# Optimization experiments

Measured on AMD Instinct MI355X. Metric: run time of the kernel, lower is better.

The kernel has to match this reference:

```python
import jax, jax.numpy as jnp
import numpy as np


def setup_inputs() -> dict:
    key = jax.random.key(0)
    nX, time_steps, T = 1024, 256, 10
    u0 = jax.random.normal(key, (nX, nX), dtype=jnp.float32)
    # learnable scalar diffusivity; 2e-4 keeps gamma <= 0.25 (stable scheme)
    alpha = jnp.asarray(2e-4, dtype=jnp.float32)
    return {"u0": u0, "alpha": alpha, "T": T, "nX": nX, "time_steps": time_steps}


def reference(u0, alpha, T, nX, time_steps):
    delta_x = 6.0 / (nX - 1)
    delta_t = T / (time_steps - 1)
    gamma = alpha * delta_t / delta_x ** 2

    # Torch code writes u0 at t=0, then zeroes all four boundaries for every t.
    u_init = jnp.zeros_like(u0).at[1:-1, 1:-1].set(u0[1:-1, 1:-1])

    def step(u, _):
        # 5-point Laplacian stencil on the interior; boundaries stay 0
        lap = (u[2:, 1:-1] + u[:-2, 1:-1] + u[1:-1, 2:] + u[1:-1, :-2]
               - 4.0 * u[1:-1, 1:-1])
        un = jnp.zeros_like(u).at[1:-1, 1:-1].set(gamma * lap + u[1:-1, 1:-1])
        return un, un

    _, us = jax.lax.scan(step, u_init, None, length=time_steps - 1)
    # u: [time_steps, nX, nX]
    return jnp.concatenate([u_init[None], us], axis=0)
```

## Files before the change

kernel.cpp:

```cpp
#include <hip/hip_runtime.h>
#include <math.h>


#define CORE 64
#define HALO 20
#define TILE 104
#define TPB  1024
#define NQ   26
#define NIT  (102 * NQ)

#define BAR() do { \
    asm volatile("s_waitcnt lgkmcnt(0)" ::: "memory"); \
    __builtin_amdgcn_s_barrier(); \
    __builtin_amdgcn_sched_barrier(0); \
} while (0)

__device__ __forceinline__ float4 load_quad_strict(const float* __restrict__ fp,
                                                   int gr, int gc0, int nX) {
    float4 v = make_float4(0.f, 0.f, 0.f, 0.f);
    if (gr > 0 && gr < nX - 1) {
        const float* sp = fp + (size_t)gr * nX + gc0;
        if (gc0 > 0 && gc0 + 3 < nX - 1) {
            v = *reinterpret_cast<const float4*>(sp);
        } else {
            if (gc0     > 0 && gc0     < nX - 1) v.x = sp[0];
            if (gc0 + 1 > 0 && gc0 + 1 < nX - 1) v.y = sp[1];
            if (gc0 + 2 > 0 && gc0 + 2 < nX - 1) v.z = sp[2];
            if (gc0 + 3 > 0 && gc0 + 3 < nX - 1) v.w = sp[3];
        }
    }
    return v;
}

__device__ __forceinline__ void slot_init(int it, int o_r, int o_c, int nX,
                                          int& a, int& off, bool& st, float4& m,
                                          int& margin) {
    const int r = 1 + it / NQ;
    const int q = it % NQ;
    a = r * TILE + 4 * q;
    const int gr  = o_r + r;
    const int gc0 = o_c + 4 * q;
    off = gr * nX + gc0;
    st  = (r >= HALO && r < HALO + CORE && q >= HALO / 4 && q < (TILE - HALO) / 4);
    const bool rin = (gr > 0 && gr < nX - 1);
    m.x = (rin && gc0     > 0 && gc0     < nX - 1) ? 1.f : 0.f;
    m.y = (rin && gc0 + 1 > 0 && gc0 + 1 < nX - 1) ? 1.f : 0.f;
    m.z = (rin && gc0 + 2 > 0 && gc0 + 2 < nX - 1) ? 1.f : 0.f;
    m.w = (rin && gc0 + 3 > 0 && gc0 + 3 < nX - 1) ? 1.f : 0.f;
    margin = min(min(r - 1, 102 - r), min(4 * q + 2, 102 - 4 * q));
}

__device__ __forceinline__ void step_one(const float* __restrict__ bc,
                                         float* __restrict__ bn,
                                         float* __restrict__ of,
                                         int a, int off, bool st,
                                         const float4& m, float4& c, float gamma) {
    const float4 u4 = *reinterpret_cast<const float4*>(bc + a - TILE);
    const float4 d4 = *reinterpret_cast<const float4*>(bc + a + TILE);
    const float lf = bc[a - 1];
    const float rt = bc[a + 4];
    float4 o;
    o.x = m.x * (c.x + gamma * (u4.x + d4.x + lf  + c.y - 4.f * c.x));
    o.y = m.y * (c.y + gamma * (u4.y + d4.y + c.x + c.z - 4.f * c.y));
    o.z = m.z * (c.z + gamma * (u4.z + d4.z + c.y + c.w - 4.f * c.z));
    o.w = m.w * (c.w + gamma * (u4.w + d4.w + c.z + rt  - 4.f * c.w));
    *reinterpret_cast<float4*>(bn + a) = o;
    if (st) *reinterpret_cast<float4*>(of + off) = o;
    c = o;
}

__global__ __launch_bounds__(TPB)
void heat_fused(const float* __restrict__ src,
                float* __restrict__ out,
                int t_base, int k, int nX, int first,
                int time_steps,
                const float* __restrict__ alpha_p,
                const int* __restrict__ T_p) {
    __shared__ float buf[2][TILE * TILE];

    const int tid = threadIdx.x;
    const int gb  = nX / CORE;
    const int bx  = blockIdx.x % gb;
    const int by  = blockIdx.x / gb;
    const int o_r = by * CORE - HALO;
    const int o_c = bx * CORE - HALO;
    const size_t n0 = (size_t)nX * nX;

    const float alpha = *alpha_p;
    const float Tf    = (float)(*T_p);
    const float dx    = 6.0f / (float)(nX - 1);
    const float dt    = Tf / (float)(time_steps - 1);
    const float gamma = alpha * dt / (dx * dx);

    for (int qi = tid; qi < TILE * NQ; qi += TPB) {
        const int r = qi / NQ, q = qi % NQ;
        const int gr = o_r + r, gc0 = o_c + 4 * q;
        const float4 v = load_quad_strict(src, gr, gc0, nX);
        *reinterpret_cast<float4*>(&buf[0][r * TILE + 4 * q]) = v;
        if (first && r >= HALO && r < HALO + CORE &&
            q >= HALO / 4 && q < (TILE - HALO) / 4)
            *reinterpret_cast<float4*>(out + (size_t)gr * nX + gc0) = v;
    }
    BAR();

    int a0, a1, a2 = TILE, off0, off1, off2 = 0, mg0, mg1, mg2 = -1;
    bool st0, st1, st2 = false;
    float4 m0, m1, m2 = make_float4(0.f, 0.f, 0.f, 0.f);
    slot_init(tid,       o_r, o_c, nX, a0, off0, st0, m0, mg0);
    slot_init(tid + TPB, o_r, o_c, nX, a1, off1, st1, m1, mg1);
    const bool has2 = (tid + 2 * TPB) < NIT;
    if (has2) slot_init(tid + 2 * TPB, o_r, o_c, nX, a2, off2, st2, m2, mg2);

    float4 c0 = *reinterpret_cast<const float4*>(&buf[0][a0]);
    float4 c1 = *reinterpret_cast<const float4*>(&buf[0][a1]);
    float4 c2 = make_float4(0.f, 0.f, 0.f, 0.f);
    if (has2) c2 = *reinterpret_cast<const float4*>(&buf[0][a2]);

    for (int s = 0; s < k; ++s) {
        const float* __restrict__ bc = buf[s & 1];
        float*       __restrict__ bn = buf[(s & 1) ^ 1];
        float* of = out + (size_t)(t_base + s + 1) * n0;

        if (s <= mg0) step_one(bc, bn, of, a0, off0, st0, m0, c0, gamma);
        if (s <= mg1) step_one(bc, bn, of, a1, off1, st1, m1, c1, gamma);
        if (s <= mg2) step_one(bc, bn, of, a2, off2, st2, m2, c2, gamma);

        BAR();
    }
}

extern "C" void kernel_launch(void* const* d_in, const int* in_sizes, int n_in,
                              void* d_out, int out_size, void* d_ws, size_t ws_size,
                              hipStream_t stream) {
    const float* u0      = (const float*)d_in[0];
    const float* alpha_p = (const float*)d_in[1];
    const int*   T_p     = (const int*)d_in[2];

    const int n0 = in_sizes[0];
    const int nX = (int)(sqrtf((float)n0) + 0.5f);
    const int ts = out_size / n0;

    float* out = (float*)d_out;
    const int gb = nX / CORE;
    const int nblocks = gb * gb;

    for (int t = 0; t < ts - 1; t += HALO) {
        const int k = min(HALO, ts - 1 - t);
        const float* src = (t == 0) ? u0 : out + (size_t)t * n0;
        heat_fused<<<nblocks, TPB, 0, stream>>>(src, out, t, k, nX,
                                                (t == 0) ? 1 : 0, ts,
                                                alpha_p, T_p);
    }
}
```

Measured before the change: 276.6 us.

## Assign 4-row vertical bands per thread and widen temporal halo to 24

```diff
diff --git a/kernel.cpp b/kernel.cpp
--- a/kernel.cpp
+++ b/kernel.cpp
@@ -3,11 +3,12 @@
 
 
 #define CORE 64
-#define HALO 20
-#define TILE 104
+#define HALO 24
+#define TILE 112
 #define TPB  1024
-#define NQ   26
-#define NIT  (102 * NQ)
+#define NQ   28
+#define NBANDS 28
+#define NUNITS (NBANDS * NQ)
 
 #define BAR() do { \
     asm volatile("s_waitcnt lgkmcnt(0)" ::: "memory"); \
@@ -32,41 +33,25 @@
     return v;
 }
 
-__device__ __forceinline__ void slot_init(int it, int o_r, int o_c, int nX,
-                                          int& a, int& off, bool& st, float4& m,
-                                          int& margin) {
-    const int r = 1 + it / NQ;
-    const int q = it % NQ;
-    a = r * TILE + 4 * q;
-    const int gr  = o_r + r;
-    const int gc0 = o_c + 4 * q;
-    off = gr * nX + gc0;
-    st  = (r >= HALO && r < HALO + CORE && q >= HALO / 4 && q < (TILE - HALO) / 4);
+__device__ __forceinline__ float4 mask_of(int gr, int gc0, int nX) {
+    float4 m;
     const bool rin = (gr > 0 && gr < nX - 1);
     m.x = (rin && gc0     > 0 && gc0     < nX - 1) ? 1.f : 0.f;
     m.y = (rin && gc0 + 1 > 0 && gc0 + 1 < nX - 1) ? 1.f : 0.f;
     m.z = (rin && gc0 + 2 > 0 && gc0 + 2 < nX - 1) ? 1.f : 0.f;
     m.w = (rin && gc0 + 3 > 0 && gc0 + 3 < nX - 1) ? 1.f : 0.f;
-    margin = min(min(r - 1, 102 - r), min(4 * q + 2, 102 - 4 * q));
+    return m;
 }
 
-__device__ __forceinline__ void step_one(const float* __restrict__ bc,
-                                         float* __restrict__ bn,
-                                         float* __restrict__ of,
-                                         int a, int off, bool st,
-                                         const float4& m, float4& c, float gamma) {
-    const float4 u4 = *reinterpret_cast<const float4*>(bc + a - TILE);
-    const float4 d4 = *reinterpret_cast<const float4*>(bc + a + TILE);
-    const float lf = bc[a - 1];
-    const float rt = bc[a + 4];
+__device__ __forceinline__ float4 stencil(const float4& c, const float4& up,
+                                          const float4& dn, float lf, float rt,
+                                          const float4& m, float gamma) {
     float4 o;
-    o.x = m.x * (c.x + gamma * (u4.x + d4.x + lf  + c.y - 4.f * c.x));
-    o.y = m.y * (c.y + gamma * (u4.y + d4.y + c.x + c.z - 4.f * c.y));
-    o.z = m.z * (c.z + gamma * (u4.z + d4.z + c.y + c.w - 4.f * c.z));
-    o.w = m.w * (c.w + gamma * (u4.w + d4.w + c.z + rt  - 4.f * c.w));
-    *reinterpret_cast<float4*>(bn + a) = o;
-    if (st) *reinterpret_cast<float4*>(of + off) = o;
-    c = o;
+    o.x = m.x * (c.x + gamma * (up.x + dn.x + lf  + c.y - 4.f * c.x));
+    o.y = m.y * (c.y + gamma * (up.y + dn.y + c.x + c.z - 4.f * c.y));
+    o.z = m.z * (c.z + gamma * (up.z + dn.z + c.y + c.w - 4.f * c.z));
+    o.w = m.w * (c.w + gamma * (up.w + dn.w + c.z + rt  - 4.f * c.w));
+    return o;
 }
 
 __global__ __launch_bounds__(TPB)
@@ -103,28 +88,74 @@
     }
     BAR();
 
-    int a0, a1, a2 = TILE, off0, off1, off2 = 0, mg0, mg1, mg2 = -1;
-    bool st0, st1, st2 = false;
-    float4 m0, m1, m2 = make_float4(0.f, 0.f, 0.f, 0.f);
-    slot_init(tid,       o_r, o_c, nX, a0, off0, st0, m0, mg0);
-    slot_init(tid + TPB, o_r, o_c, nX, a1, off1, st1, m1, mg1);
-    const bool has2 = (tid + 2 * TPB) < NIT;
-    if (has2) slot_init(tid + 2 * TPB, o_r, o_c, nX, a2, off2, st2, m2, mg2);
+    const bool hasU = tid < NUNITS;
+    const int band = tid / NQ;
+    const int q    = tid % NQ;
+    const int r0   = 1 + 4 * band;
+    const int a0   = r0 * TILE + 4 * q;
+    const int gc0  = o_c + 4 * q;
+    const int off  = (o_r + r0) * nX + gc0;
+    const bool qc  = (q >= HALO / 4 && q < (TILE - HALO) / 4);
+    const int colm = min(4 * q + 2, 110 - 4 * q);
 
-    float4 c0 = *reinterpret_cast<const float4*>(&buf[0][a0]);
-    float4 c1 = *reinterpret_cast<const float4*>(&buf[0][a1]);
-    float4 c2 = make_float4(0.f, 0.f, 0.f, 0.f);
-    if (has2) c2 = *reinterpret_cast<const float4*>(&buf[0][a2]);
+    int  mg[4];  bool st[4];  float4 m[4];
+    #pragma unroll
+    for (int i = 0; i < 4; ++i) {
+        const int rr = r0 + i;
+        mg[i] = hasU ? min(min(rr - 1, 110 - rr), colm) : -1;
+        st[i] = (rr >= HALO && rr < HALO + CORE && qc);
+        m[i]  = mask_of(o_r + rr, gc0, nX);
+    }
+    const int mgU = max(max(mg[0], mg[1]), max(mg[2], mg[3]));
+
+    float4 c0, c1, c2, c3;
+    const float4 z4 = make_float4(0.f, 0.f, 0.f, 0.f);
+    c0 = (mg[0] >= 0) ? *reinterpret_cast<const float4*>(&buf[0][a0])            : z4;
+    c1 = (mg[1] >= 0) ? *reinterpret_cast<const float4*>(&buf[0][a0 + TILE])     : z4;
+    c2 = (mg[2] >= 0) ? *reinterpret_cast<const float4*>(&buf[0][a0 + 2 * TILE]) : z4;
+    c3 = (mg[3] >= 0) ? *reinterpret_cast<const float4*>(&buf[0][a0 + 3 * TILE]) : z4;
 
     for (int s = 0; s < k; ++s) {
         const float* __restrict__ bc = buf[s & 1];
         float*       __restrict__ bn = buf[(s & 1) ^ 1];
         float* of = out + (size_t)(t_base + s + 1) * n0;
 
-        if (s <= mg0) step_one(bc, bn, of, a0, off0, st0, m0, c0, gamma);
-        if (s <= mg1) step_one(bc, bn, of, a1, off1, st1, m1, c1, gamma);
-        if (s <= mg2) step_one(bc, bn, of, a2, off2, st2, m2, c2, gamma);
-
+        if (s <= mgU) {
+            const float4 oc0 = c0, oc1 = c1, oc2 = c2, oc3 = c3;
+            if (s <= mg[0]) {
+                const float4 u4 = *reinterpret_cast<const float4*>(bc + a0 - TILE);
+                const float4 o = stencil(oc0, u4, oc1, bc[a0 - 1], bc[a0 + 4],
+                                         m[0], gamma);
+                *reinterpret_cast<float4*>(bn + a0) = o;
+                if (st[0]) *reinterpret_cast<float4*>(of + off) = o;
+                c0 = o;
+            }
+            if (s <= mg[1]) {
+                const int a = a0 + TILE;
+                const float4 o = stencil(oc1, oc0, oc2, bc[a - 1], bc[a + 4],
+                                         m[1], gamma);
+                *reinterpret_cast<float4*>(bn + a) = o;
+                if (st[1]) *reinterpret_cast<float4*>(of + off + nX) = o;
+                c1 = o;
+            }
+            if (s <= mg[2]) {
+                const int a = a0 + 2 * TILE;
+                const float4 o = stencil(oc2, oc1, oc3, bc[a - 1], bc[a + 4],
+                                         m[2], gamma);
+                *reinterpret_cast<float4*>(bn + a) = o;
+                if (st[2]) *reinterpret_cast<float4*>(of + off + 2 * nX) = o;
+                c2 = o;
+            }
+            if (s <= mg[3]) {
+                const int a = a0 + 3 * TILE;
+                const float4 d4 = *reinterpret_cast<const float4*>(bc + a + TILE);
+                const float4 o = stencil(oc3, oc2, d4, bc[a - 1], bc[a + 4],
+                                         m[3], gamma);
+                *reinterpret_cast<float4*>(bn + a) = o;
+                if (st[3]) *reinterpret_cast<float4*>(of + off + 3 * nX) = o;
+                c3 = o;
+            }
+        }
         BAR();
     }
 }
```

Result: no change. 280.0 us (+1.2%).
